# Performance work log

Hardware: AMD Instinct MI355X
Metric: run time of the kernel (lower is better)

Reference implementation:

```python
import jax, jax.numpy as jnp
import numpy as np

L = 5  # history window (init kwarg)

def _mlp(x, W1, b1, W2, b2, W3, b3):
    h = jax.nn.relu(x @ W1 + b1)
    h = jax.nn.relu(h @ W2 + b2)
    return h @ W3 + b3

def setup_inputs() -> dict:
    key = jax.random.key(0)
    ks = jax.random.split(key, 12)
    N, T1, S, D, H, E = 2000, 11, 5, 64, 256, 100000
    IN = 2 * D + 2 * L * S + 3 + 1 + 1  # 183
    return {
        "features": jax.random.normal(ks[0], (N, D), jnp.float32),
        "states": jax.random.uniform(ks[1], (N, T1, S), jnp.float32),
        "distances": jax.random.uniform(ks[2], (N, N), jnp.float32),
        "W1": jax.random.normal(ks[3], (IN, H), jnp.float32) * 0.05,
        "b1": jnp.zeros((H,), jnp.float32),
        "W2": jax.random.normal(ks[4], (H, H), jnp.float32) * 0.05,
        "b2": jnp.zeros((H,), jnp.float32),
        "W3": jax.random.normal(ks[5], (H, 3), jnp.float32) * 0.05,
        "b3": jnp.zeros((3,), jnp.float32),
        "pairs_i": jax.random.randint(ks[6], (E,), 0, N, jnp.int32),
        "pairs_j": jax.random.randint(ks[7], (E,), 0, N, jnp.int32),
        "max_timestep": 10,
    }

def reference(features, states, distances, W1, b1, W2, b2, W3, b3, pairs_i, pairs_j, max_timestep):
    T = int(max_timestep)  # static
    N, T1, S = states.shape
    E = pairs_i.shape[0]
    # --- state histories: hist[t, n] = states[n, max(0,t-L+1)..t] zero-padded, flattened to L*S
    pad = jnp.pad(states, ((0, 0), (L - 1, 0), (0, 0)))  # [N, T1+L-1, S]
    idx = jnp.arange(T + 1)[:, None] + jnp.arange(L)[None, :]  # [T+1, L]
    hist = pad[:, idx, :]  # [N, T+1, L, S]
    hist = jnp.transpose(hist, (1, 0, 2, 3)).reshape(T + 1, N, L * S)
    hist = jax.lax.stop_gradient(hist)  # original .detach()

    fi = features[pairs_i]              # [E, D]
    fj = features[pairs_j]              # [E, D]
    dist = distances[pairs_i, pairs_j][:, None]  # [E, 1]
    eye3 = jnp.eye(3, dtype=features.dtype)

    # --- t = 0: is_initial=1, dummy prev type = onehot(0); same conditional for all k_prev
    x0 = jnp.concatenate([
        fi, fj, hist[0, pairs_i], hist[0, pairs_j],
        jnp.broadcast_to(eye3[0], (E, 3)), dist, jnp.ones_like(dist)
    ], axis=-1)
    p0 = jax.nn.softmax(_mlp(x0, W1, b1, W2, b2, W3, b3), axis=-1)  # [E, 3]
    cond0 = jnp.broadcast_to(p0[:, None, :], (E, 3, 3))              # [E, 3, 3]
    m0 = p0

    # --- t >= 1: one NN call on 3 stacked prev-type branches, then forward-algo recursion
    hp_i = hist[1:, pairs_i]  # [T, E, L*S]
    hp_j = hist[1:, pairs_j]
    prev3 = jnp.broadcast_to(eye3[:, None, :], (3, E, 3))
    tail = jnp.concatenate([dist, jnp.zeros_like(dist)], axis=-1)  # [E, 2] (dist, is_initial=0)

    def step(m_prev, xs):
        hi, hj = xs
        base = jnp.concatenate([fi, fj, hi, hj], axis=-1)  # [E, 2D+2LS]
        x = jnp.concatenate([
            jnp.broadcast_to(base[None], (3, E, base.shape[-1])),
            prev3,
            jnp.broadcast_to(tail[None], (3, E, 2)),
        ], axis=-1)  # [3, E, IN]
        probs = jax.nn.softmax(_mlp(x, W1, b1, W2, b2, W3, b3), axis=-1)  # [3, E, 3]
        cond = jnp.transpose(probs, (1, 0, 2))  # [E, k_prev, k_next]
        m = jnp.einsum('ek,ekn->en', m_prev, cond)
        return m, (cond, m)

    _, (conds, margs) = jax.lax.scan(step, m0, (hp_i, hp_j))
    conditionals = jnp.concatenate([cond0[None], conds], axis=0)  # [T+1, E, 3, 3]
    marginals = jnp.concatenate([m0[None], margs], axis=0)        # [T+1, E, 3]
    return conditionals, marginals
```

## Files before the change

### kernel.cpp

```cpp
#include <hip/hip_runtime.h>
#include <hip/hip_bf16.h>
#include <math.h>

#define D_F   64
#define IN_F  183
#define KS1   6
#define KS2   8
#define HID   256
#define XPITCH 200
#define HPITCH 264
#define BM    64
#define BLK   512

typedef unsigned short u16;
typedef __attribute__((ext_vector_type(8))) short bf16x8;
typedef __attribute__((ext_vector_type(4))) float f32x4;

__device__ __forceinline__ u16 f2bf(float v) {
    __hip_bfloat16 h = __float2bfloat16(v);
    u16 u; __builtin_memcpy(&u, &h, 2); return u;
}

__global__ void pack_w_kernel(const float* __restrict__ W, u16* __restrict__ Wp,
                              int K, int KSs)
{
    int g = blockIdx.x * 256 + threadIdx.x;
    int total = 16 * KSs * 64;
    if (g >= total) return;
    int lane = g & 63;
    int ks   = (g >> 6) % KSs;
    int ct   = (g >> 6) / KSs;
    int col  = ct * 16 + (lane & 15);
    int kb   = ks * 32 + 8 * (lane >> 4);
    u16 out[8];
    #pragma unroll
    for (int j = 0; j < 8; ++j) {
        int k = kb + j;
        out[j] = f2bf((k < K) ? W[(size_t)k * HID + col] : 0.0f);
    }
    *(bf16x8*)(Wp + (size_t)g * 8) = *(const bf16x8*)out;
}

__global__ void pack_w3_kernel(const float* __restrict__ W3, u16* __restrict__ W3p)
{
    int g = blockIdx.x * 256 + threadIdx.x;
    if (g >= KS2 * 64) return;
    int lane = g & 63;
    int ks   = g >> 6;
    int n    = lane & 15;
    int kb   = ks * 32 + 8 * (lane >> 4);
    u16 out[8];
    #pragma unroll
    for (int j = 0; j < 8; ++j)
        out[j] = f2bf((n < 3) ? W3[(size_t)(kb + j) * 3 + n] : 0.0f);
    *(bf16x8*)(W3p + (size_t)g * 8) = *(const bf16x8*)out;
}

__global__ __launch_bounds__(BLK)
void mfp_mlp_mfma(const float* __restrict__ features,
                  const float* __restrict__ states,
                  const float* __restrict__ distances,
                  const float* __restrict__ W1,
                  const u16* __restrict__ W1p, const float* __restrict__ b1,
                  const u16* __restrict__ W2p, const float* __restrict__ b2,
                  const u16* __restrict__ W3p, const float* __restrict__ b3,
                  const int* __restrict__ pairs_i, const int* __restrict__ pairs_j,
                  float* __restrict__ cond,
                  int N, int T1s, int E, int T)
{
    extern __shared__ char smem[];
    u16* hsA = (u16*)smem;
    u16* hsB = hsA + BM * HPITCH;
    __shared__ int   s_pi[BM], s_pj[BM], s_e[BM], s_val[BM];
    __shared__ float s_dist[BM];

    const int tid = threadIdx.x;
    const int t   = blockIdx.y;
    const int nk  = (t == 0) ? 1 : 3;

    if (tid < BM) {
        int pe = blockIdx.x * BM + tid;
        int valid = (pe < E) ? 1 : 0;
        int e = valid ? pe : 0;
        int pi = pairs_i[e], pj = pairs_j[e];
        s_e[tid] = e; s_val[tid] = valid; s_pi[tid] = pi; s_pj[tid] = pj;
        s_dist[tid] = distances[(long long)pi * N + pj];
    }
    __syncthreads();

    u16* xs = hsA;
    for (int idx = tid; idx < BM * 32; idx += BLK) {
        int m = idx >> 5;
        int q = idx & 31;
        int src = (q < 16) ? s_pi[m] : s_pj[m];
        int c4  = (q & 15) * 4;
        float4 f = *(const float4*)&features[(size_t)src * D_F + c4];
        int c = ((q < 16) ? 0 : 64) + c4;
        ushort4 o;
        o.x = f2bf(f.x); o.y = f2bf(f.y); o.z = f2bf(f.z); o.w = f2bf(f.w);
        *(ushort4*)(xs + m * XPITCH + c) = o;
    }
    for (int idx = tid; idx < BM * 64; idx += BLK) {
        int m = idx >> 6;
        int c = 128 + (idx & 63);
        float v;
        if (c < 178) {
            int cc = c - 128;
            int row = (cc < 25) ? s_pi[m] : s_pj[m];
            int c2  = (cc < 25) ? cc : (cc - 25);
            int l = c2 / 5;
            int s = c2 - l * 5;
            int tau = t - 4 + l;
            v = (tau >= 0) ? states[((size_t)row * T1s + tau) * 5 + s] : 0.0f;
        } else if (c == 181) {
            v = s_dist[m];
        } else if (c == 182) {
            v = (t == 0) ? 1.0f : 0.0f;
        } else {
            v = 0.0f;
        }
        xs[m * XPITCH + c] = f2bf(v);
    }
    __syncthreads();

    const int lane = tid & 63;
    const int w    = tid >> 6;
    const int lr   = lane & 15;
    const int lg   = lane >> 4;

    f32x4 acc1[4][2];
    #pragma unroll
    for (int a = 0; a < 4; ++a)
        #pragma unroll
        for (int b = 0; b < 2; ++b)
            acc1[a][b] = (f32x4){0.f, 0.f, 0.f, 0.f};

    for (int ks = 0; ks < KS1; ++ks) {
        bf16x8 bfr[2];
        #pragma unroll
        for (int cl = 0; cl < 2; ++cl)
            bfr[cl] = *(const bf16x8*)(W1p + (((size_t)(2 * w + cl) * KS1 + ks) * 64 + lane) * 8);
        bf16x8 afr[4];
        #pragma unroll
        for (int rt = 0; rt < 4; ++rt)
            afr[rt] = *(const bf16x8*)(xs + (rt * 16 + lr) * XPITCH + ks * 32 + 8 * lg);
        #pragma unroll
        for (int rt = 0; rt < 4; ++rt)
            #pragma unroll
            for (int cl = 0; cl < 2; ++cl)
                acc1[rt][cl] = __builtin_amdgcn_mfma_f32_16x16x32_bf16(afr[rt], bfr[cl], acc1[rt][cl], 0, 0, 0);
    }

    float b1v[2], b2v[2], w1oh[3][2];
    #pragma unroll
    for (int cl = 0; cl < 2; ++cl) {
        int col = (2 * w + cl) * 16 + lr;
        b1v[cl] = b1[col];
        b2v[cl] = b2[col];
        #pragma unroll
        for (int k3 = 0; k3 < 3; ++k3)
            w1oh[k3][cl] = W1[(size_t)(178 + k3) * HID + col];
    }
    const float b30 = b3[0], b31 = b3[1], b32 = b3[2];

    for (int k = 0; k < nk; ++k) {
        __syncthreads();

        #pragma unroll
        for (int rt = 0; rt < 4; ++rt)
            #pragma unroll
            for (int cl = 0; cl < 2; ++cl)
                #pragma unroll
                for (int r = 0; r < 4; ++r) {
                    float h = fmaxf(acc1[rt][cl][r] + b1v[cl] + w1oh[k][cl], 0.0f);
                    hsA[(rt * 16 + 4 * lg + r) * HPITCH + (2 * w + cl) * 16 + lr] = f2bf(h);
                }
        __syncthreads();

        f32x4 acc2[4][2];
        #pragma unroll
        for (int a = 0; a < 4; ++a)
            #pragma unroll
            for (int b = 0; b < 2; ++b)
                acc2[a][b] = (f32x4){0.f, 0.f, 0.f, 0.f};

        for (int ks = 0; ks < KS2; ++ks) {
            bf16x8 bfr[2];
            #pragma unroll
            for (int cl = 0; cl < 2; ++cl)
                bfr[cl] = *(const bf16x8*)(W2p + (((size_t)(2 * w + cl) * KS2 + ks) * 64 + lane) * 8);
            bf16x8 afr[4];
            #pragma unroll
            for (int rt = 0; rt < 4; ++rt)
                afr[rt] = *(const bf16x8*)(hsA + (rt * 16 + lr) * HPITCH + ks * 32 + 8 * lg);
            #pragma unroll
            for (int rt = 0; rt < 4; ++rt)
                #pragma unroll
                for (int cl = 0; cl < 2; ++cl)
                    acc2[rt][cl] = __builtin_amdgcn_mfma_f32_16x16x32_bf16(afr[rt], bfr[cl], acc2[rt][cl], 0, 0, 0);
        }

        #pragma unroll
        for (int rt = 0; rt < 4; ++rt)
            #pragma unroll
            for (int cl = 0; cl < 2; ++cl)
                #pragma unroll
                for (int r = 0; r < 4; ++r) {
                    float g = fmaxf(acc2[rt][cl][r] + b2v[cl], 0.0f);
                    hsB[(rt * 16 + 4 * lg + r) * HPITCH + (2 * w + cl) * 16 + lr] = f2bf(g);
                }
        __syncthreads();

        if (w < 4) {
            f32x4 acc3 = (f32x4){0.f, 0.f, 0.f, 0.f};
            for (int ks = 0; ks < KS2; ++ks) {
                bf16x8 afr = *(const bf16x8*)(hsB + (16 * w + lr) * HPITCH + ks * 32 + 8 * lg);
                bf16x8 bfr = *(const bf16x8*)(W3p + ((size_t)(ks * 64 + lane)) * 8);
                acc3 = __builtin_amdgcn_mfma_f32_16x16x32_bf16(afr, bfr, acc3, 0, 0, 0);
            }
            #pragma unroll
            for (int r = 0; r < 4; ++r) {
                float l0 = acc3[r];
                float l1 = __shfl_xor(acc3[r], 1, 64);
                float l2 = __shfl_xor(acc3[r], 2, 64);
                int m = 16 * w + 4 * lg + r;
                if (lr == 0 && s_val[m]) {
                    l0 += b30; l1 += b31; l2 += b32;
                    float mx = fmaxf(l0, fmaxf(l1, l2));
                    float e0 = expf(l0 - mx), e1 = expf(l1 - mx), e2 = expf(l2 - mx);
                    float inv = 1.0f / (e0 + e1 + e2);
                    float p0 = e0 * inv, p1 = e1 * inv, p2 = e2 * inv;
                    size_t base = ((size_t)t * E + s_e[m]) * 9;
                    if (t == 0) {
                        #pragma unroll
                        for (int kb = 0; kb < 3; ++kb) {
                            cond[base + kb * 3 + 0] = p0;
                            cond[base + kb * 3 + 1] = p1;
                            cond[base + kb * 3 + 2] = p2;
                        }
                    } else {
                        cond[base + k * 3 + 0] = p0;
                        cond[base + k * 3 + 1] = p1;
                        cond[base + k * 3 + 2] = p2;
                    }
                }
            }
        }
    }
}

__global__ __launch_bounds__(256)
void mfp_marg_kernel(const float* __restrict__ cond,
                     float* __restrict__ marg,
                     int E, int T)
{
    int e = blockIdx.x * 256 + threadIdx.x;
    if (e >= E) return;
    const float* c0 = &cond[(size_t)e * 9];
    float m0 = c0[0], m1 = c0[1], m2 = c0[2];
    marg[(size_t)e * 3 + 0] = m0;
    marg[(size_t)e * 3 + 1] = m1;
    marg[(size_t)e * 3 + 2] = m2;
    for (int t = 1; t <= T; ++t) {
        const float* c9 = &cond[((size_t)t * E + e) * 9];
        float n0 = m0 * c9[0] + m1 * c9[3] + m2 * c9[6];
        float n1 = m0 * c9[1] + m1 * c9[4] + m2 * c9[7];
        float n2 = m0 * c9[2] + m1 * c9[5] + m2 * c9[8];
        m0 = n0; m1 = n1; m2 = n2;
        float* mo = &marg[((size_t)t * E + e) * 3];
        mo[0] = m0; mo[1] = m1; mo[2] = m2;
    }
}

extern "C" void kernel_launch(void* const* d_in, const int* in_sizes, int n_in,
                              void* d_out, int out_size, void* d_ws, size_t ws_size,
                              hipStream_t stream) {
    const float* features  = (const float*)d_in[0];
    const float* states    = (const float*)d_in[1];
    const float* distances = (const float*)d_in[2];
    const float* W1 = (const float*)d_in[3];
    const float* b1 = (const float*)d_in[4];
    const float* W2 = (const float*)d_in[5];
    const float* b2 = (const float*)d_in[6];
    const float* W3 = (const float*)d_in[7];
    const float* b3 = (const float*)d_in[8];
    const int* pairs_i = (const int*)d_in[9];
    const int* pairs_j = (const int*)d_in[10];

    const int N   = in_sizes[0] / D_F;
    const int T1s = in_sizes[1] / (N * 5);
    const int E   = in_sizes[9];
    const int T   = out_size / (12 * E) - 1;

    float* cond = (float*)d_out;
    float* marg = (float*)d_out + (size_t)(T + 1) * E * 9;

    u16* W1p = (u16*)d_ws;
    u16* W2p = W1p + 16 * KS1 * 64 * 8;
    u16* W3p = W2p + 16 * KS2 * 64 * 8;

    {
        int g1 = 16 * KS1 * 64;
        int g2 = 16 * KS2 * 64;
        int g3 = KS2 * 64;
        pack_w_kernel<<<(g1 + 255) / 256, 256, 0, stream>>>(W1, W1p, IN_F, KS1);
        pack_w_kernel<<<(g2 + 255) / 256, 256, 0, stream>>>(W2, W2p, HID, KS2);
        pack_w3_kernel<<<(g3 + 255) / 256, 256, 0, stream>>>(W3, W3p);
    }

    dim3 grid((E + BM - 1) / BM, T + 1);
    const size_t lds_bytes = (size_t)2 * BM * HPITCH * sizeof(u16);

    mfp_mlp_mfma<<<grid, BLK, lds_bytes, stream>>>(
        features, states, distances, W1, W1p, b1, W2p, b2, W3p, b3,
        pairs_i, pairs_j, cond, N, T1s, E, T);

    mfp_marg_kernel<<<(E + 255) / 256, 256, 0, stream>>>(cond, marg, E, T);
}
```

Baseline: 1.032 ms.

## Swap MFMA operand roles to compute transposed tiles and pack LDS writes

The MFMA operands are swapped so weights act as the A operand and activations as B. Each lane's accumulator then holds four consecutive hidden units for one row, so activations can be written to LDS as packed ushort4 instead of scattered 16-bit stores. The second LDS buffer is dropped, with layer-2 output reusing the first buffer after an extra barrier, which halves dynamic LDS and may raise occupancy. Bias and one-hot loads become vectorized, and the softmax now reads three logits from one lane instead of using shuffles.

New measurement: 886.8 us. -14.0%, faster.

```diff
diff --git a/kernel.cpp b/kernel.cpp
--- a/kernel.cpp
+++ b/kernel.cpp
@@ -7,7 +7,6 @@
 #define KS1   6
 #define KS2   8
 #define HID   256
-#define XPITCH 200
 #define HPITCH 264
 #define BM    64
 #define BLK   512
@@ -70,7 +69,6 @@
 {
     extern __shared__ char smem[];
     u16* hsA = (u16*)smem;
-    u16* hsB = hsA + BM * HPITCH;
     __shared__ int   s_pi[BM], s_pj[BM], s_e[BM], s_val[BM];
     __shared__ float s_dist[BM];
 
@@ -98,7 +96,7 @@
         int c = ((q < 16) ? 0 : 64) + c4;
         ushort4 o;
         o.x = f2bf(f.x); o.y = f2bf(f.y); o.z = f2bf(f.z); o.w = f2bf(f.w);
-        *(ushort4*)(xs + m * XPITCH + c) = o;
+        *(ushort4*)(xs + m * HPITCH + c) = o;
     }
     for (int idx = tid; idx < BM * 64; idx += BLK) {
         int m = idx >> 6;
@@ -119,7 +117,7 @@
         } else {
             v = 0.0f;
         }
-        xs[m * XPITCH + c] = f2bf(v);
+        xs[m * HPITCH + c] = f2bf(v);
     }
     __syncthreads();
 
@@ -128,121 +126,124 @@
     const int lr   = lane & 15;
     const int lg   = lane >> 4;
 
-    f32x4 acc1[4][2];
+    f32x4 acc1[2][4];
     #pragma unroll
-    for (int a = 0; a < 4; ++a)
-        #pragma unroll
-        for (int b = 0; b < 2; ++b)
+    for (int a = 0; a < 2; ++a)
+        #pragma unroll
+        for (int b = 0; b < 4; ++b)
             acc1[a][b] = (f32x4){0.f, 0.f, 0.f, 0.f};
 
     for (int ks = 0; ks < KS1; ++ks) {
-        bf16x8 bfr[2];
-        #pragma unroll
-        for (int cl = 0; cl < 2; ++cl)
-            bfr[cl] = *(const bf16x8*)(W1p + (((size_t)(2 * w + cl) * KS1 + ks) * 64 + lane) * 8);
-        bf16x8 afr[4];
-        #pragma unroll
-        for (int rt = 0; rt < 4; ++rt)
-            afr[rt] = *(const bf16x8*)(xs + (rt * 16 + lr) * XPITCH + ks * 32 + 8 * lg);
-        #pragma unroll
-        for (int rt = 0; rt < 4; ++rt)
-            #pragma unroll
-            for (int cl = 0; cl < 2; ++cl)
-                acc1[rt][cl] = __builtin_amdgcn_mfma_f32_16x16x32_bf16(afr[rt], bfr[cl], acc1[rt][cl], 0, 0, 0);
-    }
-
-    float b1v[2], b2v[2], w1oh[3][2];
+        bf16x8 wfr[2];
+        #pragma unroll
+        for (int mtl = 0; mtl < 2; ++mtl)
+            wfr[mtl] = *(const bf16x8*)(W1p + (((size_t)(2 * w + mtl) * KS1 + ks) * 64 + lane) * 8);
+        bf16x8 xfr[4];
+        #pragma unroll
+        for (int nt = 0; nt < 4; ++nt)
+            xfr[nt] = *(const bf16x8*)(xs + (nt * 16 + lr) * HPITCH + ks * 32 + 8 * lg);
+        #pragma unroll
+        for (int mtl = 0; mtl < 2; ++mtl)
+            #pragma unroll
+            for (int nt = 0; nt < 4; ++nt)
+                acc1[mtl][nt] = __builtin_amdgcn_mfma_f32_16x16x32_bf16(wfr[mtl], xfr[nt], acc1[mtl][nt], 0, 0, 0);
+    }
+
+    f32x4 b1q[2], b2q[2];
     #pragma unroll
-    for (int cl = 0; cl < 2; ++cl) {
-        int col = (2 * w + cl) * 16 + lr;
-        b1v[cl] = b1[col];
-        b2v[cl] = b2[col];
-        #pragma unroll
-        for (int k3 = 0; k3 < 3; ++k3)
-            w1oh[k3][cl] = W1[(size_t)(178 + k3) * HID + col];
+    for (int mtl = 0; mtl < 2; ++mtl) {
+        int h0 = 16 * (2 * w + mtl) + 4 * lg;
+        b1q[mtl] = *(const f32x4*)&b1[h0];
+        b2q[mtl] = *(const f32x4*)&b2[h0];
     }
     const float b30 = b3[0], b31 = b3[1], b32 = b3[2];
 
     for (int k = 0; k < nk; ++k) {
+        f32x4 ohq[2];
+        #pragma unroll
+        for (int mtl = 0; mtl < 2; ++mtl)
+            ohq[mtl] = *(const f32x4*)&W1[(size_t)(178 + k) * HID + 16 * (2 * w + mtl) + 4 * lg];
+
         __syncthreads();
 
         #pragma unroll
-        for (int rt = 0; rt < 4; ++rt)
-            #pragma unroll
-            for (int cl = 0; cl < 2; ++cl)
+        for (int mtl = 0; mtl < 2; ++mtl)
+            #pragma unroll
+            for (int nt = 0; nt < 4; ++nt) {
+                ushort4 p;
+                p.x = f2bf(fmaxf(acc1[mtl][nt][0] + b1q[mtl][0] + ohq[mtl][0], 0.0f));
+                p.y = f2bf(fmaxf(acc1[mtl][nt][1] + b1q[mtl][1] + ohq[mtl][1], 0.0f));
+                p.z = f2bf(fmaxf(acc1[mtl][nt][2] + b1q[mtl][2] + ohq[mtl][2], 0.0f));
+                p.w = f2bf(fmaxf(acc1[mtl][nt][3] + b1q[mtl][3] + ohq[mtl][3], 0.0f));
+                *(ushort4*)(hsA + (nt * 16 + lr) * HPITCH + 16 * (2 * w + mtl) + 4 * lg) = p;
+            }
+        __syncthreads();
+
+        f32x4 acc2[2][4];
+        #pragma unroll
+        for (int a = 0; a < 2; ++a)
+            #pragma unroll
+            for (int b = 0; b < 4; ++b)
+                acc2[a][b] = (f32x4){0.f, 0.f, 0.f, 0.f};
+
+        for (int ks = 0; ks < KS2; ++ks) {
+            bf16x8 wfr[2];
+            #pragma unroll
+            for (int mtl = 0; mtl < 2; ++mtl)
+                wfr[mtl] = *(const bf16x8*)(W2p + (((size_t)(2 * w + mtl) * KS2 + ks) * 64 + lane) * 8);
+            bf16x8 hfr[4];
+            #pragma unroll
+            for (int nt = 0; nt < 4; ++nt)
+                hfr[nt] = *(const bf16x8*)(hsA + (nt * 16 + lr) * HPITCH + ks * 32 + 8 * lg);
+            #pragma unroll
+            for (int mtl = 0; mtl < 2; ++mtl)
                 #pragma unroll
-                for (int r = 0; r < 4; ++r) {
-                    float h = fmaxf(acc1[rt][cl][r] + b1v[cl] + w1oh[k][cl], 0.0f);
-                    hsA[(rt * 16 + 4 * lg + r) * HPITCH + (2 * w + cl) * 16 + lr] = f2bf(h);
-                }
+                for (int nt = 0; nt < 4; ++nt)
+                    acc2[mtl][nt] = __builtin_amdgcn_mfma_f32_16x16x32_bf16(wfr[mtl], hfr[nt], acc2[mtl][nt], 0, 0, 0);
+        }
         __syncthreads();
 
-        f32x4 acc2[4][2];
-        #pragma unroll
-        for (int a = 0; a < 4; ++a)
-            #pragma unroll
-            for (int b = 0; b < 2; ++b)
-                acc2[a][b] = (f32x4){0.f, 0.f, 0.f, 0.f};
-
-        for (int ks = 0; ks < KS2; ++ks) {
-            bf16x8 bfr[2];
-            #pragma unroll
-            for (int cl = 0; cl < 2; ++cl)
-                bfr[cl] = *(const bf16x8*)(W2p + (((size_t)(2 * w + cl) * KS2 + ks) * 64 + lane) * 8);
-            bf16x8 afr[4];
-            #pragma unroll
-            for (int rt = 0; rt < 4; ++rt)
-                afr[rt] = *(const bf16x8*)(hsA + (rt * 16 + lr) * HPITCH + ks * 32 + 8 * lg);
-            #pragma unroll
-            for (int rt = 0; rt < 4; ++rt)
-                #pragma unroll
-                for (int cl = 0; cl < 2; ++cl)
-                    acc2[rt][cl] = __builtin_amdgcn_mfma_f32_16x16x32_bf16(afr[rt], bfr[cl], acc2[rt][cl], 0, 0, 0);
-        }
-
-        #pragma unroll
-        for (int rt = 0; rt < 4; ++rt)
-            #pragma unroll
-            for (int cl = 0; cl < 2; ++cl)
-                #pragma unroll
-                for (int r = 0; r < 4; ++r) {
-                    float g = fmaxf(acc2[rt][cl][r] + b2v[cl], 0.0f);
-                    hsB[(rt * 16 + 4 * lg + r) * HPITCH + (2 * w + cl) * 16 + lr] = f2bf(g);
-                }
+        #pragma unroll
+        for (int mtl = 0; mtl < 2; ++mtl)
+            #pragma unroll
+            for (int nt = 0; nt < 4; ++nt) {
+                ushort4 p;
+                p.x = f2bf(fmaxf(acc2[mtl][nt][0] + b2q[mtl][0], 0.0f));
+                p.y = f2bf(fmaxf(acc2[mtl][nt][1] + b2q[mtl][1], 0.0f));
+                p.z = f2bf(fmaxf(acc2[mtl][nt][2] + b2q[mtl][2], 0.0f));
+                p.w = f2bf(fmaxf(acc2[mtl][nt][3] + b2q[mtl][3], 0.0f));
+                *(ushort4*)(hsA + (nt * 16 + lr) * HPITCH + 16 * (2 * w + mtl) + 4 * lg) = p;
+            }
         __syncthreads();
 
         if (w < 4) {
             f32x4 acc3 = (f32x4){0.f, 0.f, 0.f, 0.f};
             for (int ks = 0; ks < KS2; ++ks) {
-                bf16x8 afr = *(const bf16x8*)(hsB + (16 * w + lr) * HPITCH + ks * 32 + 8 * lg);
-                bf16x8 bfr = *(const bf16x8*)(W3p + ((size_t)(ks * 64 + lane)) * 8);
-                acc3 = __builtin_amdgcn_mfma_f32_16x16x32_bf16(afr, bfr, acc3, 0, 0, 0);
+                bf16x8 hfr = *(const bf16x8*)(hsA + (w * 16 + lr) * HPITCH + ks * 32 + 8 * lg);
+                bf16x8 wfr = *(const bf16x8*)(W3p + ((size_t)(ks * 64 + lane)) * 8);
+                acc3 = __builtin_amdgcn_mfma_f32_16x16x32_bf16(wfr, hfr, acc3, 0, 0, 0);
             }
-            #pragma unroll
-            for (int r = 0; r < 4; ++r) {
-                float l0 = acc3[r];
-                float l1 = __shfl_xor(acc3[r], 1, 64);
-                float l2 = __shfl_xor(acc3[r], 2, 64);
-                int m = 16 * w + 4 * lg + r;
-                if (lr == 0 && s_val[m]) {
-                    l0 += b30; l1 += b31; l2 += b32;
-                    float mx = fmaxf(l0, fmaxf(l1, l2));
-                    float e0 = expf(l0 - mx), e1 = expf(l1 - mx), e2 = expf(l2 - mx);
-                    float inv = 1.0f / (e0 + e1 + e2);
-                    float p0 = e0 * inv, p1 = e1 * inv, p2 = e2 * inv;
-                    size_t base = ((size_t)t * E + s_e[m]) * 9;
-                    if (t == 0) {
-                        #pragma unroll
-                        for (int kb = 0; kb < 3; ++kb) {
-                            cond[base + kb * 3 + 0] = p0;
-                            cond[base + kb * 3 + 1] = p1;
-                            cond[base + kb * 3 + 2] = p2;
-                        }
-                    } else {
-                        cond[base + k * 3 + 0] = p0;
-                        cond[base + k * 3 + 1] = p1;
-                        cond[base + k * 3 + 2] = p2;
+            int m = 16 * w + lr;
+            if (lg == 0 && s_val[m]) {
+                float l0 = acc3[0] + b30;
+                float l1 = acc3[1] + b31;
+                float l2 = acc3[2] + b32;
+                float mx = fmaxf(l0, fmaxf(l1, l2));
+                float e0 = expf(l0 - mx), e1 = expf(l1 - mx), e2 = expf(l2 - mx);
+                float inv = 1.0f / (e0 + e1 + e2);
+                float p0 = e0 * inv, p1 = e1 * inv, p2 = e2 * inv;
+                size_t base = ((size_t)t * E + s_e[m]) * 9;
+                if (t == 0) {
+                    #pragma unroll
+                    for (int kb = 0; kb < 3; ++kb) {
+                        cond[base + kb * 3 + 0] = p0;
+                        cond[base + kb * 3 + 1] = p1;
+                        cond[base + kb * 3 + 2] = p2;
                     }
+                } else {
+                    cond[base + k * 3 + 0] = p0;
+                    cond[base + k * 3 + 1] = p1;
+                    cond[base + k * 3 + 2] = p2;
                 }
             }
         }
@@ -309,7 +310,7 @@
     }
 
     dim3 grid((E + BM - 1) / BM, T + 1);
-    const size_t lds_bytes = (size_t)2 * BM * HPITCH * sizeof(u16);
+    const size_t lds_bytes = (size_t)BM * HPITCH * sizeof(u16);
 
     mfp_mlp_mfma<<<grid, BLK, lds_bytes, stream>>>(
         features, states, distances, W1, W1p, b1, W2p, b2, W3p, b3,
```

## Swap MFMA operands and fuse layer-3 projection into layer-2 epilogue

Applied to the files above, without the earlier changes.

The GEMMs now use weights as the A operand and activations as the B operand, so each lane holds four consecutive hidden units and can write them as packed ushort4 stores with vectorised bias loads. The third layer is no longer an MFMA over a second LDS buffer. It is computed in fp32 inside the layer-2 epilogue using W3 held in shared memory, reduced across lanes with shuffles and across waves through a small LDS array. This removes the hsB buffer, one barrier-separated phase per branch, and the W3 packing kernel, which halves dynamic LDS and may improve occupancy. The cost is extra shuffles and an LDS reduction.

Result: no change. 1.034 ms (+0.3%).

```diff
diff --git a/kernel.cpp b/kernel.cpp
--- a/kernel.cpp
+++ b/kernel.cpp
@@ -7,7 +7,6 @@
 #define KS1   6
 #define KS2   8
 #define HID   256
-#define XPITCH 200
 #define HPITCH 264
 #define BM    64
 #define BLK   512
@@ -29,8 +28,8 @@
     if (g >= total) return;
     int lane = g & 63;
     int ks   = (g >> 6) % KSs;
-    int ct   = (g >> 6) / KSs;
-    int col  = ct * 16 + (lane & 15);
+    int mt   = (g >> 6) / KSs;
+    int col  = mt * 16 + (lane & 15);
     int kb   = ks * 32 + 8 * (lane >> 4);
     u16 out[8];
     #pragma unroll
@@ -39,21 +38,6 @@
         out[j] = f2bf((k < K) ? W[(size_t)k * HID + col] : 0.0f);
     }
     *(bf16x8*)(Wp + (size_t)g * 8) = *(const bf16x8*)out;
-}
-
-__global__ void pack_w3_kernel(const float* __restrict__ W3, u16* __restrict__ W3p)
-{
-    int g = blockIdx.x * 256 + threadIdx.x;
-    if (g >= KS2 * 64) return;
-    int lane = g & 63;
-    int ks   = g >> 6;
-    int n    = lane & 15;
-    int kb   = ks * 32 + 8 * (lane >> 4);
-    u16 out[8];
-    #pragma unroll
-    for (int j = 0; j < 8; ++j)
-        out[j] = f2bf((n < 3) ? W3[(size_t)(kb + j) * 3 + n] : 0.0f);
-    *(bf16x8*)(W3p + (size_t)g * 8) = *(const bf16x8*)out;
 }
 
 __global__ __launch_bounds__(BLK)
@@ -63,16 +47,17 @@
                   const float* __restrict__ W1,
                   const u16* __restrict__ W1p, const float* __restrict__ b1,
                   const u16* __restrict__ W2p, const float* __restrict__ b2,
-                  const u16* __restrict__ W3p, const float* __restrict__ b3,
+                  const float* __restrict__ W3, const float* __restrict__ b3,
                   const int* __restrict__ pairs_i, const int* __restrict__ pairs_j,
                   float* __restrict__ cond,
                   int N, int T1s, int E, int T)
 {
     extern __shared__ char smem[];
     u16* hsA = (u16*)smem;
-    u16* hsB = hsA + BM * HPITCH;
     __shared__ int   s_pi[BM], s_pj[BM], s_e[BM], s_val[BM];
     __shared__ float s_dist[BM];
+    __shared__ float s_w3[HID][4];
+    __shared__ float s_plog[4][BM][3];
 
     const int tid = threadIdx.x;
     const int t   = blockIdx.y;
@@ -85,6 +70,10 @@
         int pi = pairs_i[e], pj = pairs_j[e];
         s_e[tid] = e; s_val[tid] = valid; s_pi[tid] = pi; s_pj[tid] = pj;
         s_dist[tid] = distances[(long long)pi * N + pj];
+    }
+    for (int idx = tid; idx < HID * 4; idx += BLK) {
+        int h = idx >> 2, n = idx & 3;
+        s_w3[h][n] = (n < 3) ? W3[h * 3 + n] : 0.0f;
     }
     __syncthreads();
 
@@ -98,7 +87,7 @@
         int c = ((q < 16) ? 0 : 64) + c4;
         ushort4 o;
         o.x = f2bf(f.x); o.y = f2bf(f.y); o.z = f2bf(f.z); o.w = f2bf(f.w);
-        *(ushort4*)(xs + m * XPITCH + c) = o;
+        *(ushort4*)(xs + m * HPITCH + c) = o;
     }
     for (int idx = tid; idx < BM * 64; idx += BLK) {
         int m = idx >> 6;
@@ -119,131 +108,144 @@
         } else {
             v = 0.0f;
         }
-        xs[m * XPITCH + c] = f2bf(v);
+        xs[m * HPITCH + c] = f2bf(v);
     }
     __syncthreads();
 
     const int lane = tid & 63;
     const int w    = tid >> 6;
+    const int a    = w & 3;
+    const int b    = w >> 2;
     const int lr   = lane & 15;
     const int lg   = lane >> 4;
 
     f32x4 acc1[4][2];
     #pragma unroll
-    for (int a = 0; a < 4; ++a)
-        #pragma unroll
-        for (int b = 0; b < 2; ++b)
-            acc1[a][b] = (f32x4){0.f, 0.f, 0.f, 0.f};
+    for (int i = 0; i < 4; ++i)
+        #pragma unroll
+        for (int j = 0; j < 2; ++j)
+            acc1[i][j] = (f32x4){0.f, 0.f, 0.f, 0.f};
 
     for (int ks = 0; ks < KS1; ++ks) {
-        bf16x8 bfr[2];
-        #pragma unroll
-        for (int cl = 0; cl < 2; ++cl)
-            bfr[cl] = *(const bf16x8*)(W1p + (((size_t)(2 * w + cl) * KS1 + ks) * 64 + lane) * 8);
-        bf16x8 afr[4];
-        #pragma unroll
-        for (int rt = 0; rt < 4; ++rt)
-            afr[rt] = *(const bf16x8*)(xs + (rt * 16 + lr) * XPITCH + ks * 32 + 8 * lg);
-        #pragma unroll
-        for (int rt = 0; rt < 4; ++rt)
-            #pragma unroll
-            for (int cl = 0; cl < 2; ++cl)
-                acc1[rt][cl] = __builtin_amdgcn_mfma_f32_16x16x32_bf16(afr[rt], bfr[cl], acc1[rt][cl], 0, 0, 0);
-    }
-
-    float b1v[2], b2v[2], w1oh[3][2];
-    #pragma unroll
-    for (int cl = 0; cl < 2; ++cl) {
-        int col = (2 * w + cl) * 16 + lr;
-        b1v[cl] = b1[col];
-        b2v[cl] = b2[col];
-        #pragma unroll
-        for (int k3 = 0; k3 < 3; ++k3)
-            w1oh[k3][cl] = W1[(size_t)(178 + k3) * HID + col];
-    }
-    const float b30 = b3[0], b31 = b3[1], b32 = b3[2];
+        bf16x8 wfr[4];
+        #pragma unroll
+        for (int mtl = 0; mtl < 4; ++mtl)
+            wfr[mtl] = *(const bf16x8*)(W1p + (((size_t)(4 * a + mtl) * KS1 + ks) * 64 + lane) * 8);
+        bf16x8 xfr[2];
+        #pragma unroll
+        for (int ntl = 0; ntl < 2; ++ntl)
+            xfr[ntl] = *(const bf16x8*)(xs + (32 * b + 16 * ntl + lr) * HPITCH + ks * 32 + 8 * lg);
+        #pragma unroll
+        for (int mtl = 0; mtl < 4; ++mtl)
+            #pragma unroll
+            for (int ntl = 0; ntl < 2; ++ntl)
+                acc1[mtl][ntl] = __builtin_amdgcn_mfma_f32_16x16x32_bf16(wfr[mtl], xfr[ntl], acc1[mtl][ntl], 0, 0, 0);
+    }
 
     for (int k = 0; k < nk; ++k) {
         __syncthreads();
 
         #pragma unroll
-        for (int rt = 0; rt < 4; ++rt)
-            #pragma unroll
-            for (int cl = 0; cl < 2; ++cl)
+        for (int mtl = 0; mtl < 4; ++mtl) {
+            int h0 = 16 * (4 * a + mtl) + 4 * lg;
+            f32x4 b1q = *(const f32x4*)&b1[h0];
+            f32x4 ohq = *(const f32x4*)&W1[(size_t)(178 + k) * HID + h0];
+            #pragma unroll
+            for (int ntl = 0; ntl < 2; ++ntl) {
+                ushort4 p;
+                p.x = f2bf(fmaxf(acc1[mtl][ntl][0] + b1q[0] + ohq[0], 0.0f));
+                p.y = f2bf(fmaxf(acc1[mtl][ntl][1] + b1q[1] + ohq[1], 0.0f));
+                p.z = f2bf(fmaxf(acc1[mtl][ntl][2] + b1q[2] + ohq[2], 0.0f));
+                p.w = f2bf(fmaxf(acc1[mtl][ntl][3] + b1q[3] + ohq[3], 0.0f));
+                *(ushort4*)(hsA + (32 * b + 16 * ntl + lr) * HPITCH + h0) = p;
+            }
+        }
+        __syncthreads();
+
+        f32x4 acc2[4][2];
+        #pragma unroll
+        for (int i = 0; i < 4; ++i)
+            #pragma unroll
+            for (int j = 0; j < 2; ++j)
+                acc2[i][j] = (f32x4){0.f, 0.f, 0.f, 0.f};
+
+        for (int ks = 0; ks < KS2; ++ks) {
+            bf16x8 wfr[4];
+            #pragma unroll
+            for (int mtl = 0; mtl < 4; ++mtl)
+                wfr[mtl] = *(const bf16x8*)(W2p + (((size_t)(4 * a + mtl) * KS2 + ks) * 64 + lane) * 8);
+            bf16x8 hfr[2];
+            #pragma unroll
+            for (int ntl = 0; ntl < 2; ++ntl)
+                hfr[ntl] = *(const bf16x8*)(hsA + (32 * b + 16 * ntl + lr) * HPITCH + ks * 32 + 8 * lg);
+            #pragma unroll
+            for (int mtl = 0; mtl < 4; ++mtl)
+                #pragma unroll
+                for (int ntl = 0; ntl < 2; ++ntl)
+                    acc2[mtl][ntl] = __builtin_amdgcn_mfma_f32_16x16x32_bf16(wfr[mtl], hfr[ntl], acc2[mtl][ntl], 0, 0, 0);
+        }
+
+        float part[2][3];
+        part[0][0] = 0.f; part[0][1] = 0.f; part[0][2] = 0.f;
+        part[1][0] = 0.f; part[1][1] = 0.f; part[1][2] = 0.f;
+
+        #pragma unroll
+        for (int mtl = 0; mtl < 4; ++mtl) {
+            int h0 = 16 * (4 * a + mtl) + 4 * lg;
+            f32x4 b2q = *(const f32x4*)&b2[h0];
+            f32x4 w3r[4];
+            #pragma unroll
+            for (int r = 0; r < 4; ++r)
+                w3r[r] = *(const f32x4*)&s_w3[h0 + r][0];
+            #pragma unroll
+            for (int ntl = 0; ntl < 2; ++ntl)
                 #pragma unroll
                 for (int r = 0; r < 4; ++r) {
-                    float h = fmaxf(acc1[rt][cl][r] + b1v[cl] + w1oh[k][cl], 0.0f);
-                    hsA[(rt * 16 + 4 * lg + r) * HPITCH + (2 * w + cl) * 16 + lr] = f2bf(h);
+                    float h2 = fmaxf(acc2[mtl][ntl][r] + b2q[r], 0.0f);
+                    part[ntl][0] = fmaf(h2, w3r[r][0], part[ntl][0]);
+                    part[ntl][1] = fmaf(h2, w3r[r][1], part[ntl][1]);
+                    part[ntl][2] = fmaf(h2, w3r[r][2], part[ntl][2]);
                 }
+        }
+        #pragma unroll
+        for (int ntl = 0; ntl < 2; ++ntl)
+            #pragma unroll
+            for (int n = 0; n < 3; ++n) {
+                part[ntl][n] += __shfl_xor(part[ntl][n], 16, 64);
+                part[ntl][n] += __shfl_xor(part[ntl][n], 32, 64);
+            }
+        if (lg == 0) {
+            #pragma unroll
+            for (int ntl = 0; ntl < 2; ++ntl) {
+                int m = 32 * b + 16 * ntl + lr;
+                s_plog[a][m][0] = part[ntl][0];
+                s_plog[a][m][1] = part[ntl][1];
+                s_plog[a][m][2] = part[ntl][2];
+            }
+        }
         __syncthreads();
 
-        f32x4 acc2[4][2];
-        #pragma unroll
-        for (int a = 0; a < 4; ++a)
-            #pragma unroll
-            for (int b = 0; b < 2; ++b)
-                acc2[a][b] = (f32x4){0.f, 0.f, 0.f, 0.f};
-
-        for (int ks = 0; ks < KS2; ++ks) {
-            bf16x8 bfr[2];
-            #pragma unroll
-            for (int cl = 0; cl < 2; ++cl)
-                bfr[cl] = *(const bf16x8*)(W2p + (((size_t)(2 * w + cl) * KS2 + ks) * 64 + lane) * 8);
-            bf16x8 afr[4];
-            #pragma unroll
-            for (int rt = 0; rt < 4; ++rt)
-                afr[rt] = *(const bf16x8*)(hsA + (rt * 16 + lr) * HPITCH + ks * 32 + 8 * lg);
-            #pragma unroll
-            for (int rt = 0; rt < 4; ++rt)
+        if (tid < BM && s_val[tid]) {
+            int m = tid;
+            float l0 = s_plog[0][m][0] + s_plog[1][m][0] + s_plog[2][m][0] + s_plog[3][m][0] + b3[0];
+            float l1 = s_plog[0][m][1] + s_plog[1][m][1] + s_plog[2][m][1] + s_plog[3][m][1] + b3[1];
+            float l2 = s_plog[0][m][2] + s_plog[1][m][2] + s_plog[2][m][2] + s_plog[3][m][2] + b3[2];
+            float mx = fmaxf(l0, fmaxf(l1, l2));
+            float e0 = expf(l0 - mx), e1 = expf(l1 - mx), e2 = expf(l2 - mx);
+            float inv = 1.0f / (e0 + e1 + e2);
+            float p0 = e0 * inv, p1 = e1 * inv, p2 = e2 * inv;
+            size_t base = ((size_t)t * E + s_e[m]) * 9;
+            if (t == 0) {
                 #pragma unroll
-                for (int cl = 0; cl < 2; ++cl)
-                    acc2[rt][cl] = __builtin_amdgcn_mfma_f32_16x16x32_bf16(afr[rt], bfr[cl], acc2[rt][cl], 0, 0, 0);
-        }
-
-        #pragma unroll
-        for (int rt = 0; rt < 4; ++rt)
-            #pragma unroll
-            for (int cl = 0; cl < 2; ++cl)
-                #pragma unroll
-                for (int r = 0; r < 4; ++r) {
-                    float g = fmaxf(acc2[rt][cl][r] + b2v[cl], 0.0f);
-                    hsB[(rt * 16 + 4 * lg + r) * HPITCH + (2 * w + cl) * 16 + lr] = f2bf(g);
+                for (int kb = 0; kb < 3; ++kb) {
+                    cond[base + kb * 3 + 0] = p0;
+                    cond[base + kb * 3 + 1] = p1;
+                    cond[base + kb * 3 + 2] = p2;
                 }
-        __syncthreads();
-
-        if (w < 4) {
-            f32x4 acc3 = (f32x4){0.f, 0.f, 0.f, 0.f};
-            for (int ks = 0; ks < KS2; ++ks) {
-                bf16x8 afr = *(const bf16x8*)(hsB + (16 * w + lr) * HPITCH + ks * 32 + 8 * lg);
-                bf16x8 bfr = *(const bf16x8*)(W3p + ((size_t)(ks * 64 + lane)) * 8);
-                acc3 = __builtin_amdgcn_mfma_f32_16x16x32_bf16(afr, bfr, acc3, 0, 0, 0);
-            }
-            #pragma unroll
-            for (int r = 0; r < 4; ++r) {
-                float l0 = acc3[r];
-                float l1 = __shfl_xor(acc3[r], 1, 64);
-                float l2 = __shfl_xor(acc3[r], 2, 64);
-                int m = 16 * w + 4 * lg + r;
-                if (lr == 0 && s_val[m]) {
-                    l0 += b30; l1 += b31; l2 += b32;
-                    float mx = fmaxf(l0, fmaxf(l1, l2));
-                    float e0 = expf(l0 - mx), e1 = expf(l1 - mx), e2 = expf(l2 - mx);
-                    float inv = 1.0f / (e0 + e1 + e2);
-                    float p0 = e0 * inv, p1 = e1 * inv, p2 = e2 * inv;
-                    size_t base = ((size_t)t * E + s_e[m]) * 9;
-                    if (t == 0) {
-                        #pragma unroll
-                        for (int kb = 0; kb < 3; ++kb) {
-                            cond[base + kb * 3 + 0] = p0;
-                            cond[base + kb * 3 + 1] = p1;
-                            cond[base + kb * 3 + 2] = p2;
-                        }
-                    } else {
-                        cond[base + k * 3 + 0] = p0;
-                        cond[base + k * 3 + 1] = p1;
-                        cond[base + k * 3 + 2] = p2;
-                    }
-                }
+            } else {
+                cond[base + k * 3 + 0] = p0;
+                cond[base + k * 3 + 1] = p1;
+                cond[base + k * 3 + 2] = p2;
             }
         }
     }
@@ -297,22 +299,19 @@
 
     u16* W1p = (u16*)d_ws;
     u16* W2p = W1p + 16 * KS1 * 64 * 8;
-    u16* W3p = W2p + 16 * KS2 * 64 * 8;
 
     {
         int g1 = 16 * KS1 * 64;
         int g2 = 16 * KS2 * 64;
-        int g3 = KS2 * 64;
         pack_w_kernel<<<(g1 + 255) / 256, 256, 0, stream>>>(W1, W1p, IN_F, KS1);
         pack_w_kernel<<<(g2 + 255) / 256, 256, 0, stream>>>(W2, W2p, HID, KS2);
-        pack_w3_kernel<<<(g3 + 255) / 256, 256, 0, stream>>>(W3, W3p);
     }
 
     dim3 grid((E + BM - 1) / BM, T + 1);
-    const size_t lds_bytes = (size_t)2 * BM * HPITCH * sizeof(u16);
+    const size_t lds_bytes = (size_t)BM * HPITCH * sizeof(u16);
 
     mfp_mlp_mfma<<<grid, BLK, lds_bytes, stream>>>(
-        features, states, distances, W1, W1p, b1, W2p, b2, W3p, b3,
+        features, states, distances, W1, W1p, b1, W2p, b2, W3, b3,
         pairs_i, pairs_j, cond, N, T1s, E, T);
 
     mfp_marg_kernel<<<(E + 255) / 256, 256, 0, stream>>>(cond, marg, E, T);
```
